# Kernel optimization log

Hardware: AMD Instinct MI355X
Metric: run time of the kernel (lower is better)

## Reference

```python
import jax, jax.numpy as jnp
import numpy as np

KE = 14.3996
ALPHA = 0.3
CUTOFF = 10.0
K_MAX = 6
N_ATOMS = 100000
N_PAIRS = 6400000
N_MOL = 64


def _generate_kvecs():
    kr = np.arange(0, K_MAX + 1, dtype=np.float32)
    kr = np.concatenate([kr, -kr[1:]])
    # cartesian product of (kr, kr, kr)
    g = np.stack(np.meshgrid(kr, kr, kr, indexing='ij'), axis=-1).reshape(-1, 3)
    norm = (g ** 2).sum(axis=1)
    mask = (norm <= K_MAX ** 2 + 2) & (norm != 0)
    return jnp.asarray(g[mask])  # [1020, 3]


def setup_inputs() -> dict:
    key = jax.random.key(0)
    k1, k2, k3, k4, k5, k6, k7 = jax.random.split(key, 7)
    partial_charges = jax.random.normal(k1, (N_ATOMS, 1), dtype=jnp.float32)
    # pair displacement vectors; scale so typical |r_ij| ~ 3-6 A, avoids d ~ 0
    Rij = jax.random.normal(k2, (N_PAIRS, 3), dtype=jnp.float32) * 3.0 + 1.0
    R = jax.random.uniform(k3, (N_ATOMS, 3), dtype=jnp.float32) * 20.0
    # orthorhombic-ish invertible cells: diag(~20) + small perturbation
    cell = jnp.eye(3, dtype=jnp.float32)[None] * 20.0 \
        + jax.random.uniform(k4, (N_MOL, 3, 3), dtype=jnp.float32) * 0.1
    idx_m = jnp.sort(jax.random.randint(k5, (N_ATOMS,), 0, N_MOL)).astype(jnp.int64)
    idx_i = jax.random.randint(k6, (N_PAIRS,), 0, N_ATOMS).astype(jnp.int64)
    idx_j = jax.random.randint(k7, (N_PAIRS,), 0, N_ATOMS).astype(jnp.int64)
    kvecs = _generate_kvecs()
    return {"partial_charges": partial_charges, "Rij": Rij, "R": R, "cell": cell,
            "kvecs": kvecs, "idx_m": idx_m, "idx_i": idx_i, "idx_j": idx_j}


def reference(partial_charges, Rij, R, cell, kvecs, idx_m, idx_i, idx_j):
    q = partial_charges.squeeze(-1)                      # [A]
    d_ij = jnp.linalg.norm(Rij, axis=1)                  # [P]
    sqrt_a = jnp.sqrt(jnp.float32(ALPHA))

    # ---- real space: gather q, erfc-screened pair potential, double scatter ----
    f_r = jax.scipy.special.erfc(sqrt_a * d_ij) / d_ij
    f_r_cut = jax.scipy.special.erfc(sqrt_a * CUTOFF) / CUTOFF
    pot_ij = q[idx_i] * q[idx_j] * (f_r - f_r_cut)
    pot_ij = jnp.where(d_ij <= CUTOFF, pot_ij, jnp.zeros_like(pot_ij))
    y_atom = jax.ops.segment_sum(pot_ij, idx_i, num_segments=N_ATOMS)
    y_real = 0.5 * KE * jax.ops.segment_sum(y_atom, idx_m, num_segments=N_MOL)

    # ---- reciprocal space ----
    two_pi = 2.0 * jnp.float32(np.pi)
    recip_box = two_pi * jnp.transpose(jnp.linalg.inv(cell), (0, 2, 1))  # [M,3,3]
    v_box = jnp.abs(jnp.linalg.det(cell))                                # [M]
    prefactor = two_pi / v_box
    kv = jnp.einsum('kd,mde->mke', kvecs, recip_box)     # [M,K,3]
    k_sq = jnp.sum(kv ** 2, axis=2)                      # [M,K]
    q_gauss = jnp.exp(-0.25 * k_sq / ALPHA)              # [M,K]
    # per-atom phase: gather per-molecule k-vectors, dot with positions
    kdp = jnp.einsum('akd,ad->ak', kv[idx_m], R)         # [A,K]
    q_real = jax.ops.segment_sum(q[:, None] * jnp.cos(kdp), idx_m, num_segments=N_MOL)
    q_imag = jax.ops.segment_sum(q[:, None] * jnp.sin(kdp), idx_m, num_segments=N_MOL)
    q_dens = q_real ** 2 + q_imag ** 2                   # [M,K]
    y_ewald = prefactor * jnp.sum(q_dens * q_gauss / k_sq, axis=1)
    self_int = jnp.sqrt(ALPHA / np.pi) * jax.ops.segment_sum(q ** 2, idx_m, num_segments=N_MOL)
    y_recip = KE * (y_ewald - self_int)

    return y_real + y_recip                              # [M]
```

## Files before the change

kernel.cpp:

```cpp
#include <hip/hip_runtime.h>
#include <math.h>

#define KE_C     14.3996f
#define ALPHA_C  0.3f
#define CUTOFF_C 10.0f
#define TWO_PI_C 6.283185307179586f
#define KSPL     4
#define ASPL     4
#define NRECIP   1024

typedef float vfloat4 __attribute__((ext_vector_type(4)));
typedef int   vint4   __attribute__((ext_vector_type(4)));

__device__ __forceinline__ float fast_erfc(float x) {
    float t = __builtin_amdgcn_rcpf(fmaf(0.3275911f, x, 1.0f));
    float p = fmaf(t, 1.061405429f, -1.453152027f);
    p = fmaf(t, p, 1.421413741f);
    p = fmaf(t, p, -0.284496736f);
    p = fmaf(t, p, 0.254829592f);
    return t * p * __expf(-x * x);
}

__global__ __launch_bounds__(64) void k_cell(const float* __restrict__ cell,
                                             float* __restrict__ RB,
                                             float* __restrict__ VB, int nmol) {
    int m = blockIdx.x * blockDim.x + threadIdx.x;
    if (m >= nmol) return;
    const float* c = cell + m * 9;
    float a00 = c[0], a01 = c[1], a02 = c[2];
    float a10 = c[3], a11 = c[4], a12 = c[5];
    float a20 = c[6], a21 = c[7], a22 = c[8];
    float det = a00 * (a11 * a22 - a12 * a21)
              - a01 * (a10 * a22 - a12 * a20)
              + a02 * (a10 * a21 - a11 * a20);
    float id = 1.0f / det;
    float inv00 = (a11 * a22 - a12 * a21) * id;
    float inv01 = (a02 * a21 - a01 * a22) * id;
    float inv02 = (a01 * a12 - a02 * a11) * id;
    float inv10 = (a12 * a20 - a10 * a22) * id;
    float inv11 = (a00 * a22 - a02 * a20) * id;
    float inv12 = (a02 * a10 - a00 * a12) * id;
    float inv20 = (a10 * a21 - a11 * a20) * id;
    float inv21 = (a01 * a20 - a00 * a21) * id;
    float inv22 = (a00 * a11 - a01 * a10) * id;
    float* rb = RB + m * 9;
    rb[0] = TWO_PI_C * inv00; rb[1] = TWO_PI_C * inv10; rb[2] = TWO_PI_C * inv20;
    rb[3] = TWO_PI_C * inv01; rb[4] = TWO_PI_C * inv11; rb[5] = TWO_PI_C * inv21;
    rb[6] = TWO_PI_C * inv02; rb[7] = TWO_PI_C * inv12; rb[8] = TWO_PI_C * inv22;
    VB[m] = fabsf(det);
}

__global__ __launch_bounds__(128) void k_bounds(const int* __restrict__ idx_m,
                                                int* __restrict__ bounds,
                                                int natoms, int nmol) {
    int m = threadIdx.x;
    if (m > nmol) return;
    int lo = 0, hi = natoms;
    while (lo < hi) {
        int mid = (lo + hi) >> 1;
        if (idx_m[mid] < m) lo = mid + 1; else hi = mid;
    }
    bounds[m] = lo;
}

__global__ __launch_bounds__(256) void k_atoms(const float* __restrict__ R,
                                               const float* __restrict__ q,
                                               const int* __restrict__ idx_m,
                                               const float* __restrict__ RB,
                                               float4* __restrict__ S4,
                                               float2* __restrict__ QM,
                                               float* __restrict__ SI, int natoms) {
    __shared__ float si[64];
    int tid = threadIdx.x;
    if (tid < 64) si[tid] = 0.0f;
    __syncthreads();
    int a = blockIdx.x * 256 + tid;
    if (a < natoms) {
        int m = idx_m[a];
        float r0 = R[3 * a], r1 = R[3 * a + 1], r2 = R[3 * a + 2];
        const float* rb = RB + m * 9;
        float s0 = rb[0] * r0 + rb[1] * r1 + rb[2] * r2;
        float s1 = rb[3] * r0 + rb[4] * r1 + rb[5] * r2;
        float s2 = rb[6] * r0 + rb[7] * r1 + rb[8] * r2;
        float qa = q[a];
        S4[a] = make_float4(s0, s1, s2, qa);
        QM[a] = make_float2(qa, __int_as_float(m));
        atomicAdd(&si[m & 63], qa * qa);
    }
    __syncthreads();
    if (tid < 64) atomicAdd(&SI[tid], si[tid]);
}

__global__ __launch_bounds__(256) void k_main(const float4* __restrict__ S4,
                                              const float* __restrict__ kvecs,
                                              const int* __restrict__ bounds,
                                              float* __restrict__ QR,
                                              float* __restrict__ QI, int nk,
                                              const float* __restrict__ Rij,
                                              const int* __restrict__ idx_i,
                                              const int* __restrict__ idx_j,
                                              const float2* __restrict__ QM,
                                              float* __restrict__ YRpad, int npairs) {
    __shared__ float acc[4][64];
    int tid = threadIdx.x;
    int bid = blockIdx.x;

    if (bid < NRECIP) {
        int m  = bid >> 4;
        int kc = (bid >> 2) & 3;
        int ac = bid & 3;
        int s0 = bounds[m], s1 = bounds[m + 1];
        int per = (s1 - s0 + ASPL - 1) / ASPL;
        int a0 = s0 + ac * per;
        int a1 = min(a0 + per, s1);
        int k = kc * 256 + tid;
        float kx = 0.f, ky = 0.f, kz = 0.f;
        if (k < nk) { kx = kvecs[3 * k]; ky = kvecs[3 * k + 1]; kz = kvecs[3 * k + 2]; }
        float qr = 0.f, qi = 0.f;
#pragma unroll 4
        for (int t = a0; t < a1; ++t) {
            float4 s = S4[t];
            float ph = fmaf(kx, s.x, fmaf(ky, s.y, kz * s.z));
            float sn, cs;
            __sincosf(ph, &sn, &cs);
            qr = fmaf(s.w, cs, qr);
            qi = fmaf(s.w, sn, qi);
        }
        if (k < nk) {
            atomicAdd(&QR[m * nk + k], qr);
            atomicAdd(&QI[m * nk + k], qi);
        }
    } else {
        int wave = tid >> 6;
        ((float*)acc)[tid] = 0.0f;
        __syncthreads();
        const float sqa = 0.5477225575051661f;
        const float frcut = fast_erfc(sqa * CUTOFF_C) / CUTOFF_C;
        long base = ((long)(bid - NRECIP) * 256 + tid) << 3;
        if (base + 8 <= npairs) {
            vint4 ii0 = __builtin_nontemporal_load((const vint4*)(idx_i + base));
            vint4 ii1 = __builtin_nontemporal_load((const vint4*)(idx_i + base) + 1);
            vint4 jj0 = __builtin_nontemporal_load((const vint4*)(idx_j + base));
            vint4 jj1 = __builtin_nontemporal_load((const vint4*)(idx_j + base) + 1);
            const vfloat4* r4 = (const vfloat4*)(Rij + 3 * base);
            vfloat4 A = __builtin_nontemporal_load(r4 + 0);
            vfloat4 B = __builtin_nontemporal_load(r4 + 1);
            vfloat4 C = __builtin_nontemporal_load(r4 + 2);
            vfloat4 D = __builtin_nontemporal_load(r4 + 3);
            vfloat4 E = __builtin_nontemporal_load(r4 + 4);
            vfloat4 F = __builtin_nontemporal_load(r4 + 5);
            float2 qa0 = QM[ii0.x], qa1 = QM[ii0.y], qa2 = QM[ii0.z], qa3 = QM[ii0.w];
            float2 qa4 = QM[ii1.x], qa5 = QM[ii1.y], qa6 = QM[ii1.z], qa7 = QM[ii1.w];
            float2 qb0 = QM[jj0.x], qb1 = QM[jj0.y], qb2 = QM[jj0.z], qb3 = QM[jj0.w];
            float2 qb4 = QM[jj1.x], qb5 = QM[jj1.y], qb6 = QM[jj1.z], qb7 = QM[jj1.w];
#define PAIR(xx, yy, zz, qa, qb)                                              \
            {                                                                 \
                float d2 = fmaf(xx, xx, fmaf(yy, yy, (zz) * (zz)));           \
                if (d2 <= CUTOFF_C * CUTOFF_C) {                              \
                    float rd = __builtin_amdgcn_rsqf(d2);                     \
                    float d = d2 * rd;                                        \
                    float f = fast_erfc(sqa * d) * rd - frcut;                \
                    atomicAdd(&acc[wave][__float_as_int((qa).y) & 63],        \
                              (qa).x * (qb).x * f);                           \
                }                                                             \
            }
            PAIR(A.x, A.y, A.z, qa0, qb0)
            PAIR(A.w, B.x, B.y, qa1, qb1)
            PAIR(B.z, B.w, C.x, qa2, qb2)
            PAIR(C.y, C.z, C.w, qa3, qb3)
            PAIR(D.x, D.y, D.z, qa4, qb4)
            PAIR(D.w, E.x, E.y, qa5, qb5)
            PAIR(E.z, E.w, F.x, qa6, qb6)
            PAIR(F.y, F.z, F.w, qa7, qb7)
#undef PAIR
        } else if (base < npairs) {
            for (long p = base; p < npairs; ++p) {
                float x = Rij[3 * p], y = Rij[3 * p + 1], z = Rij[3 * p + 2];
                float d2 = fmaf(x, x, fmaf(y, y, z * z));
                if (d2 <= CUTOFF_C * CUTOFF_C) {
                    float rd = __builtin_amdgcn_rsqf(d2);
                    float d = d2 * rd;
                    float2 qi2 = QM[idx_i[p]];
                    float2 qj2 = QM[idx_j[p]];
                    atomicAdd(&acc[wave][__float_as_int(qi2.y) & 63],
                              qi2.x * qj2.x * (fast_erfc(sqa * d) * rd - frcut));
                }
            }
        }
        __syncthreads();
        if (tid < 64) {
            float v = acc[0][tid] + acc[1][tid] + acc[2][tid] + acc[3][tid];
            atomicAdd(&YRpad[tid * 16], v);
        }
    }
}

__global__ __launch_bounds__(256) void k_final(const float* __restrict__ kvecs,
                                               const float* __restrict__ RB,
                                               const float* __restrict__ VB,
                                               const float* __restrict__ QR,
                                               const float* __restrict__ QI,
                                               const float* __restrict__ YRpad,
                                               const float* __restrict__ SI,
                                               float* __restrict__ out, int nk) {
    int m = blockIdx.x;
    int tid = threadIdx.x;
    __shared__ float rb[9];
    __shared__ float wsum[4];
    if (tid < 9) rb[tid] = RB[m * 9 + tid];
    __syncthreads();
    float acc = 0.0f;
    for (int k = tid; k < nk; k += 256) {
        float gx = kvecs[3 * k], gy = kvecs[3 * k + 1], gz = kvecs[3 * k + 2];
        float kv0 = gx * rb[0] + gy * rb[3] + gz * rb[6];
        float kv1 = gx * rb[1] + gy * rb[4] + gz * rb[7];
        float kv2 = gx * rb[2] + gy * rb[5] + gz * rb[8];
        float ksq = kv0 * kv0 + kv1 * kv1 + kv2 * kv2;
        float qr = QR[m * nk + k], qi = QI[m * nk + k];
        acc += (qr * qr + qi * qi) * __expf(-0.25f / ALPHA_C * ksq) / ksq;
    }
#pragma unroll
    for (int off = 32; off > 0; off >>= 1) acc += __shfl_down(acc, off, 64);
    if ((tid & 63) == 0) wsum[tid >> 6] = acc;
    __syncthreads();
    if (tid == 0) {
        float s = wsum[0] + wsum[1] + wsum[2] + wsum[3];
        float pref = TWO_PI_C / VB[m];
        float self_c = sqrtf(ALPHA_C / 3.14159265358979323846f);
        out[m] = 0.5f * KE_C * YRpad[m * 16] + KE_C * (pref * s - self_c * SI[m]);
    }
}

extern "C" void kernel_launch(void* const* d_in, const int* in_sizes, int n_in,
                              void* d_out, int out_size, void* d_ws, size_t ws_size,
                              hipStream_t stream) {
    const float* q     = (const float*)d_in[0];
    const float* Rij   = (const float*)d_in[1];
    const float* R     = (const float*)d_in[2];
    const float* cell  = (const float*)d_in[3];
    const float* kvecs = (const float*)d_in[4];
    const int*   idx_m = (const int*)d_in[5];
    const int*   idx_i = (const int*)d_in[6];
    const int*   idx_j = (const int*)d_in[7];

    int natoms = in_sizes[0];
    int npairs = in_sizes[1] / 3;
    int nmol   = in_sizes[3] / 9;
    int nk     = in_sizes[4] / 3;
    float* out = (float*)d_out;

    float* W      = (float*)d_ws;
    float* RB     = W;
    float* VB     = RB + 576;
    int*   bounds = (int*)(VB + 64);
    float4* S4    = (float4*)(W + 720);
    float2* QM    = (float2*)(W + 720 + 4 * (size_t)natoms);
    float* QR     = W + 720 + 6 * (size_t)natoms;
    float* QI     = QR + (size_t)nmol * nk;
    float* SI     = QI + (size_t)nmol * nk;
    float* YRpad  = SI + 64;

    size_t zero_bytes = ((size_t)2 * nmol * nk + 64 + 64 * 16) * sizeof(float);
    (void)hipMemsetAsync(QR, 0, zero_bytes, stream);

    int nrb = (npairs + 2047) / 2048;
    k_cell  <<<1, 64, 0, stream>>>(cell, RB, VB, nmol);
    k_bounds<<<1, 128, 0, stream>>>(idx_m, bounds, natoms, nmol);
    k_atoms <<<(natoms + 255) / 256, 256, 0, stream>>>(R, q, idx_m, RB, S4, QM, SI, natoms);
    k_main  <<<NRECIP + nrb, 256, 0, stream>>>(S4, kvecs, bounds, QR, QI, nk,
                                               Rij, idx_i, idx_j, QM, YRpad, npairs);
    k_final <<<nmol, 256, 0, stream>>>(kvecs, RB, VB, QR, QI, YRpad, SI, out, nk);
}
```

Before: 264.7 us.

## Exploit k/-k symmetry to halve reciprocal work and use native revolution sincos

Reciprocal-space structure factors are now computed only for the half of k-vectors with positive canonical sign, since |S(k)|=|S(-k)| for real charges, and the energy sum is doubled in the final kernel. Fractional coordinates are prescaled by 1/(2π) so the phase can go through fract plus the hardware sin/cos in revolutions, skipping range reduction. Each thread now handles two k-vectors, and atoms are split 32 ways per molecule instead of 4, which changes the block count and the atomic traffic. The trade-off is an extra tiny compaction kernel, and reliance on at most 512 half k-vectors, which holds for these inputs with 510 of 1020.

```diff
diff --git a/kernel.cpp b/kernel.cpp
--- a/kernel.cpp
+++ b/kernel.cpp
@@ -5,9 +5,9 @@
 #define ALPHA_C  0.3f
 #define CUTOFF_C 10.0f
 #define TWO_PI_C 6.283185307179586f
-#define KSPL     4
-#define ASPL     4
-#define NRECIP   1024
+#define INV_2PI  0.15915494309189535f
+#define ASPL     32
+#define NK2      512
 
 typedef float vfloat4 __attribute__((ext_vector_type(4)));
 typedef int   vint4   __attribute__((ext_vector_type(4)));
@@ -19,6 +19,12 @@
     p = fmaf(t, p, -0.284496736f);
     p = fmaf(t, p, 0.254829592f);
     return t * p * __expf(-x * x);
+}
+
+__device__ __forceinline__ void sincos_rev(float x, float* s, float* c) {
+    float f = __builtin_amdgcn_fractf(x);
+    *s = __builtin_amdgcn_sinf(f);
+    *c = __builtin_amdgcn_cosf(f);
 }
 
 __global__ __launch_bounds__(64) void k_cell(const float* __restrict__ cell,
@@ -63,6 +69,21 @@
     bounds[m] = lo;
 }
 
+__global__ __launch_bounds__(256) void k_khalf(const float* __restrict__ kvecs,
+                                               float4* __restrict__ KH,
+                                               int* __restrict__ cnt, int nk) {
+    int k = blockIdx.x * 256 + threadIdx.x;
+    if (k >= nk) return;
+    float gx = kvecs[3 * k], gy = kvecs[3 * k + 1], gz = kvecs[3 * k + 2];
+    bool pos = (gx > 0.5f) ||
+               (fabsf(gx) < 0.5f && (gy > 0.5f ||
+                (fabsf(gy) < 0.5f && gz > 0.5f)));
+    if (pos) {
+        int s = atomicAdd(cnt, 1);
+        KH[s] = make_float4(gx, gy, gz, 0.0f);
+    }
+}
+
 __global__ __launch_bounds__(256) void k_atoms(const float* __restrict__ R,
                                                const float* __restrict__ q,
                                                const int* __restrict__ idx_m,
@@ -79,9 +100,9 @@
         int m = idx_m[a];
         float r0 = R[3 * a], r1 = R[3 * a + 1], r2 = R[3 * a + 2];
         const float* rb = RB + m * 9;
-        float s0 = rb[0] * r0 + rb[1] * r1 + rb[2] * r2;
-        float s1 = rb[3] * r0 + rb[4] * r1 + rb[5] * r2;
-        float s2 = rb[6] * r0 + rb[7] * r1 + rb[8] * r2;
+        float s0 = (rb[0] * r0 + rb[1] * r1 + rb[2] * r2) * INV_2PI;
+        float s1 = (rb[3] * r0 + rb[4] * r1 + rb[5] * r2) * INV_2PI;
+        float s2 = (rb[6] * r0 + rb[7] * r1 + rb[8] * r2) * INV_2PI;
         float qa = q[a];
         S4[a] = make_float4(s0, s1, s2, qa);
         QM[a] = make_float2(qa, __int_as_float(m));
@@ -92,10 +113,10 @@
 }
 
 __global__ __launch_bounds__(256) void k_main(const float4* __restrict__ S4,
-                                              const float* __restrict__ kvecs,
+                                              const float4* __restrict__ KH,
                                               const int* __restrict__ bounds,
                                               float* __restrict__ QR,
-                                              float* __restrict__ QI, int nk,
+                                              float* __restrict__ QI, int nrecip,
                                               const float* __restrict__ Rij,
                                               const int* __restrict__ idx_i,
                                               const int* __restrict__ idx_j,
@@ -105,38 +126,40 @@
     int tid = threadIdx.x;
     int bid = blockIdx.x;
 
-    if (bid < NRECIP) {
-        int m  = bid >> 4;
-        int kc = (bid >> 2) & 3;
-        int ac = bid & 3;
+    if (bid < nrecip) {
+        int m  = bid / ASPL;
+        int ac = bid % ASPL;
         int s0 = bounds[m], s1 = bounds[m + 1];
         int per = (s1 - s0 + ASPL - 1) / ASPL;
         int a0 = s0 + ac * per;
         int a1 = min(a0 + per, s1);
-        int k = kc * 256 + tid;
-        float kx = 0.f, ky = 0.f, kz = 0.f;
-        if (k < nk) { kx = kvecs[3 * k]; ky = kvecs[3 * k + 1]; kz = kvecs[3 * k + 2]; }
-        float qr = 0.f, qi = 0.f;
+        float4 g0 = KH[tid];
+        float4 g1 = KH[tid + 256];
+        float qr0 = 0.f, qi0 = 0.f, qr1 = 0.f, qi1 = 0.f;
 #pragma unroll 4
         for (int t = a0; t < a1; ++t) {
             float4 s = S4[t];
-            float ph = fmaf(kx, s.x, fmaf(ky, s.y, kz * s.z));
-            float sn, cs;
-            __sincosf(ph, &sn, &cs);
-            qr = fmaf(s.w, cs, qr);
-            qi = fmaf(s.w, sn, qi);
+            float ph0 = fmaf(g0.x, s.x, fmaf(g0.y, s.y, g0.z * s.z));
+            float ph1 = fmaf(g1.x, s.x, fmaf(g1.y, s.y, g1.z * s.z));
+            float sn0, cs0, sn1, cs1;
+            sincos_rev(ph0, &sn0, &cs0);
+            sincos_rev(ph1, &sn1, &cs1);
+            qr0 = fmaf(s.w, cs0, qr0);
+            qi0 = fmaf(s.w, sn0, qi0);
+            qr1 = fmaf(s.w, cs1, qr1);
+            qi1 = fmaf(s.w, sn1, qi1);
         }
-        if (k < nk) {
-            atomicAdd(&QR[m * nk + k], qr);
-            atomicAdd(&QI[m * nk + k], qi);
-        }
+        atomicAdd(&QR[m * NK2 + tid], qr0);
+        atomicAdd(&QI[m * NK2 + tid], qi0);
+        atomicAdd(&QR[m * NK2 + tid + 256], qr1);
+        atomicAdd(&QI[m * NK2 + tid + 256], qi1);
     } else {
         int wave = tid >> 6;
         ((float*)acc)[tid] = 0.0f;
         __syncthreads();
         const float sqa = 0.5477225575051661f;
         const float frcut = fast_erfc(sqa * CUTOFF_C) / CUTOFF_C;
-        long base = ((long)(bid - NRECIP) * 256 + tid) << 3;
+        long base = ((long)(bid - nrecip) * 256 + tid) << 3;
         if (base + 8 <= npairs) {
             vint4 ii0 = __builtin_nontemporal_load((const vint4*)(idx_i + base));
             vint4 ii1 = __builtin_nontemporal_load((const vint4*)(idx_i + base) + 1);
@@ -195,28 +218,30 @@
     }
 }
 
-__global__ __launch_bounds__(256) void k_final(const float* __restrict__ kvecs,
+__global__ __launch_bounds__(256) void k_final(const float4* __restrict__ KH,
+                                               const int* __restrict__ cnt,
                                                const float* __restrict__ RB,
                                                const float* __restrict__ VB,
                                                const float* __restrict__ QR,
                                                const float* __restrict__ QI,
                                                const float* __restrict__ YRpad,
                                                const float* __restrict__ SI,
-                                               float* __restrict__ out, int nk) {
+                                               float* __restrict__ out) {
     int m = blockIdx.x;
     int tid = threadIdx.x;
     __shared__ float rb[9];
     __shared__ float wsum[4];
     if (tid < 9) rb[tid] = RB[m * 9 + tid];
     __syncthreads();
+    int nhalf = cnt[0];
     float acc = 0.0f;
-    for (int k = tid; k < nk; k += 256) {
-        float gx = kvecs[3 * k], gy = kvecs[3 * k + 1], gz = kvecs[3 * k + 2];
-        float kv0 = gx * rb[0] + gy * rb[3] + gz * rb[6];
-        float kv1 = gx * rb[1] + gy * rb[4] + gz * rb[7];
-        float kv2 = gx * rb[2] + gy * rb[5] + gz * rb[8];
+    for (int k = tid; k < nhalf; k += 256) {
+        float4 g = KH[k];
+        float kv0 = g.x * rb[0] + g.y * rb[3] + g.z * rb[6];
+        float kv1 = g.x * rb[1] + g.y * rb[4] + g.z * rb[7];
+        float kv2 = g.x * rb[2] + g.y * rb[5] + g.z * rb[8];
         float ksq = kv0 * kv0 + kv1 * kv1 + kv2 * kv2;
-        float qr = QR[m * nk + k], qi = QI[m * nk + k];
+        float qr = QR[m * NK2 + k], qi = QI[m * NK2 + k];
         acc += (qr * qr + qi * qi) * __expf(-0.25f / ALPHA_C * ksq) / ksq;
     }
 #pragma unroll
@@ -224,7 +249,7 @@
     if ((tid & 63) == 0) wsum[tid >> 6] = acc;
     __syncthreads();
     if (tid == 0) {
-        float s = wsum[0] + wsum[1] + wsum[2] + wsum[3];
+        float s = 2.0f * (wsum[0] + wsum[1] + wsum[2] + wsum[3]);
         float pref = TWO_PI_C / VB[m];
         float self_c = sqrtf(ALPHA_C / 3.14159265358979323846f);
         out[m] = 0.5f * KE_C * YRpad[m * 16] + KE_C * (pref * s - self_c * SI[m]);
@@ -249,25 +274,30 @@
     int nk     = in_sizes[4] / 3;
     float* out = (float*)d_out;
 
-    float* W      = (float*)d_ws;
-    float* RB     = W;
-    float* VB     = RB + 576;
-    int*   bounds = (int*)(VB + 64);
-    float4* S4    = (float4*)(W + 720);
-    float2* QM    = (float2*)(W + 720 + 4 * (size_t)natoms);
-    float* QR     = W + 720 + 6 * (size_t)natoms;
-    float* QI     = QR + (size_t)nmol * nk;
-    float* SI     = QI + (size_t)nmol * nk;
-    float* YRpad  = SI + 64;
-
-    size_t zero_bytes = ((size_t)2 * nmol * nk + 64 + 64 * 16) * sizeof(float);
-    (void)hipMemsetAsync(QR, 0, zero_bytes, stream);
-
+    float*  W      = (float*)d_ws;
+    float*  RB     = W;
+    float*  VB     = RB + 576;
+    int*    bounds = (int*)(VB + 64);
+    float4* S4     = (float4*)(W + 720);
+    float2* QM     = (float2*)(W + 720 + 4 * (size_t)natoms);
+    size_t  zoff   = 720 + 6 * (size_t)natoms;
+    zoff = (zoff + 3) & ~(size_t)3;
+    float4* KH     = (float4*)(W + zoff);
+    float*  QR     = W + zoff + 4 * NK2;
+    float*  QI     = QR + (size_t)nmol * NK2;
+    float*  SI     = QI + (size_t)nmol * NK2;
+    float*  YRpad  = SI + 64;
+    int*    cnt    = (int*)(YRpad + 64 * 16);
+    size_t zero_bytes = (4 * NK2 + (size_t)2 * nmol * NK2 + 64 + 64 * 16 + 4) * sizeof(float);
+    (void)hipMemsetAsync(KH, 0, zero_bytes, stream);
+
+    int nrecip = nmol * ASPL;
     int nrb = (npairs + 2047) / 2048;
     k_cell  <<<1, 64, 0, stream>>>(cell, RB, VB, nmol);
     k_bounds<<<1, 128, 0, stream>>>(idx_m, bounds, natoms, nmol);
+    k_khalf <<<(nk + 255) / 256, 256, 0, stream>>>(kvecs, KH, cnt, nk);
     k_atoms <<<(natoms + 255) / 256, 256, 0, stream>>>(R, q, idx_m, RB, S4, QM, SI, natoms);
-    k_main  <<<NRECIP + nrb, 256, 0, stream>>>(S4, kvecs, bounds, QR, QI, nk,
+    k_main  <<<nrecip + nrb, 256, 0, stream>>>(S4, KH, bounds, QR, QI, nrecip,
                                                Rij, idx_i, idx_j, QM, YRpad, npairs);
-    k_final <<<nmol, 256, 0, stream>>>(kvecs, RB, VB, QR, QI, YRpad, SI, out, nk);
-}
+    k_final <<<nmol, 256, 0, stream>>>(KH, cnt, RB, VB, QR, QI, YRpad, SI, out);
+}
```

Measured after the change: 261.6 us. No clear change (-1.2%).
